# Kernel optimization log

Hardware: AMD Instinct MI355X
Metric: run time of the kernel (lower is better)

Reference implementation:

```python
import jax, jax.numpy as jnp
import numpy as np

N = 50000      # nodes
E = 800000     # edges (avg degree 16)
F_IN = 128
# (d_in, d_out) for the 9 GCNConv layers with width=256, n_layers=3
DIMS = [(128, 128), (128, 192), (192, 256), (256, 256), (256, 256), (256, 256), (256, 192), (192, 128), (128, 1)]
# ReLU after every conv except loop conv i==n_layers-2 (conv idx 4) and the final conv
RELU = [True, True, True, True, False, True, True, True, False]


def setup_inputs() -> dict:
    key = jax.random.key(0)
    ks = jax.random.split(key, 2 + 2 * len(DIMS))
    inp = {
        "x": jax.random.normal(ks[0], (N, F_IN), dtype=jnp.float32),
        "edge_index": jax.random.randint(ks[1], (2, E), 0, N, dtype=jnp.int64),
    }
    for i, (din, dout) in enumerate(DIMS):
        # Glorot-ish init for weights, small random bias (GCNConv has bias=True)
        inp[f"W{i}"] = jax.random.normal(ks[2 + 2 * i], (din, dout), dtype=jnp.float32) / np.float32(np.sqrt(din))
        inp[f"b{i}"] = jax.random.normal(ks[3 + 2 * i], (dout,), dtype=jnp.float32) * 0.01
    return inp


def _gcn_stack(x, src_f, dst_f, norm, Ws, bs):
    h = x
    for i in range(len(Ws)):
        h = h @ Ws[i]                                  # [N, dout] dense transform first (dout <= din mostly)
        msg = h[src_f] * norm[:, None]                 # gather + edge-normalize  [E+N, dout]
        h = jax.ops.segment_sum(msg, dst_f, num_segments=N) + bs[i]
        if RELU[i]:
            h = jax.nn.relu(h)
        # Dropout layers are identity in eval/inference mode.
    return h


def reference(x, edge_index,
              W0, b0, W1, b1, W2, b2, W3, b3, W4, b4, W5, b5, W6, b6, W7, b7, W8, b8):
    src, dst = edge_index[0], edge_index[1]
    loop = jnp.arange(N, dtype=src.dtype)
    # GCNConv default: add self loops, symmetric normalization D^{-1/2}(A+I)D^{-1/2}
    src_f = jnp.concatenate([src, loop])
    dst_f = jnp.concatenate([dst, loop])
    deg = jax.ops.segment_sum(jnp.ones(E + N, dtype=x.dtype), dst_f, num_segments=N)
    dinv = jax.lax.rsqrt(jnp.maximum(deg, 1.0))        # deg >= 1 thanks to self loops
    norm = dinv[src_f] * dinv[dst_f]                   # per-edge coefficient [E+N]
    Ws = [W0, W1, W2, W3, W4, W5, W6, W7, W8]
    bs = [b0, b1, b2, b3, b4, b5, b6, b7, b8]
    return _gcn_stack(x, src_f, dst_f, norm, Ws, bs)   # [N, 1]
```

## Files before the change

### kernel.cpp

```cpp
#include <hip/hip_runtime.h>


#define TPB 256

using bf16x8 = __attribute__((ext_vector_type(8))) __bf16;
using f32x4  = __attribute__((ext_vector_type(4))) float;
using f32x2  = __attribute__((ext_vector_type(2))) float;

__device__ __forceinline__ unsigned bf16rne(float x) {
    unsigned u = __float_as_uint(x);
    return (u + 0x7fffu + ((u >> 16) & 1u)) >> 16;
}

__device__ __forceinline__ f32x2 bl2(unsigned u) {
    return (f32x2){__uint_as_float(u << 16), __uint_as_float(u & 0xffff0000u)};
}

__device__ __forceinline__ void stage16(const unsigned short* g, unsigned short* l) {
#if __has_builtin(__builtin_amdgcn_global_load_lds)
    __builtin_amdgcn_global_load_lds((const __attribute__((address_space(1))) void*)g,
                                     (__attribute__((address_space(3))) void*)l, 16, 0, 0);
#else
    *(uint4*)((char*)l + (threadIdx.x & 63) * 16) = *(const uint4*)g;
#endif
}


__global__ void zinit_kernel(int* cnt, int n) {
    int i = blockIdx.x * blockDim.x + threadIdx.x;
    if (i < n) cnt[i] = 0;
}

__global__ void count_kernel(const int* __restrict__ dst, int* __restrict__ cnt,
                             int* __restrict__ rank, int E) {
    int e = blockIdx.x * blockDim.x + threadIdx.x;
    if (e < E) rank[e] = atomicAdd(&cnt[dst[e]], 1);
}


__global__ void blockhist_kernel(const int* __restrict__ cnt, int* __restrict__ localRank,
                                 int* __restrict__ hb, float* __restrict__ dinv,
                                 int n, int nb) {
    __shared__ int h[64];
    int t = threadIdx.x;
    if (t < 64) h[t] = 0;
    __syncthreads();
    int i = blockIdx.x * TPB + t;
    if (i < n) {
        int c = cnt[i];
        dinv[i] = rsqrtf((float)(c + 1));
        int d = c; if (d > 63) d = 63;
        localRank[i] = atomicAdd(&h[d], 1);
    }
    __syncthreads();
    if (t < 64) hb[t * nb + blockIdx.x] = h[t];
}

__global__ __launch_bounds__(256) void sortscan_kernel(int* __restrict__ hb, int nb) {
    __shared__ int sh[64 * 256];
    __shared__ int tot[64], base[64];
    int t = threadIdx.x;
    int total = 64 * nb;
    for (int i = t; i < total; i += 256) sh[i] = hb[i];
    __syncthreads();
    if (t < 64) {
        int run = 0;
        for (int b = 0; b < nb; b++) {
            int v = sh[t * nb + b];
            sh[t * nb + b] = run;
            run += v;
        }
        tot[t] = run;
    }
    __syncthreads();
    if (t == 0) {
        int acc = 0;
        for (int b = 0; b < 64; b++) { base[b] = acc; acc += tot[b]; }
    }
    __syncthreads();
    for (int i = t; i < total; i += 256) hb[i] = sh[i] + base[i / nb];
}

__global__ void scatter2_kernel(const int* __restrict__ cnt,
                                const int* __restrict__ localRank, const int* __restrict__ hb,
                                int* __restrict__ perm, int* __restrict__ pcnt,
                                int* __restrict__ iperm, int n, int nb) {
    int i = blockIdx.x * TPB + threadIdx.x;
    if (i >= n) return;
    int c = cnt[i];
    int d = c; if (d > 63) d = 63;
    int pos = hb[d * nb + blockIdx.x] + localRank[i];
    perm[pos] = i;
    pcnt[pos] = c;
    iperm[i] = pos;
}

__global__ void scan1_kernel(const int* __restrict__ pcnt, int* __restrict__ prowp2,
                             int* __restrict__ bsums, int n) {
    __shared__ int sh[TPB];
    int t = threadIdx.x;
    int i = blockIdx.x * TPB + t;
    int v = (i < n) ? (pcnt[i] + 1) : 0;
    sh[t] = v;
    __syncthreads();
    for (int off = 1; off < TPB; off <<= 1) {
        int x = (t >= off) ? sh[t - off] : 0;
        __syncthreads();
        sh[t] += x;
        __syncthreads();
    }
    if (i < n) prowp2[i] = sh[t] - v;
    if (t == TPB - 1) bsums[blockIdx.x] = sh[t];
}

__global__ void scan2_kernel(int* __restrict__ bsums, int nb) {
    __shared__ int sh[TPB];
    int t = threadIdx.x;
    int v = (t < nb) ? bsums[t] : 0;
    sh[t] = v;
    __syncthreads();
    for (int off = 1; off < TPB; off <<= 1) {
        int x = (t >= off) ? sh[t - off] : 0;
        __syncthreads();
        sh[t] += x;
        __syncthreads();
    }
    if (t < nb) bsums[t] = sh[t] - v;
}

__global__ void scan3_kernel(int* __restrict__ rowp, const int* __restrict__ bsums, int n) {
    int i = blockIdx.x * TPB + threadIdx.x;
    if (i < n) rowp[i] += bsums[blockIdx.x];
}

__global__ void rowo_kernel(const int* __restrict__ iperm, const int* __restrict__ prowp2,
                            int* __restrict__ rowo, int n) {
    int i = blockIdx.x * TPB + threadIdx.x;
    if (i < n) rowo[i] = prowp2[iperm[i]];
}

__global__ void fillself_kernel(const int* __restrict__ src, const int* __restrict__ dst,
                                const int* __restrict__ rank,
                                const float* __restrict__ dinv,
                                const int* __restrict__ rowo,
                                const int* __restrict__ cnt,
                                unsigned* __restrict__ edges2, int E, int n) {
    int id = blockIdx.x * blockDim.x + threadIdx.x;
    if (id < E) {
        int s = src[id], d = dst[id];
        int pos = rowo[d] + rank[id];
        edges2[pos] = (unsigned)s | (bf16rne(dinv[s] * dinv[d]) << 16);
    } else if (id < E + n) {
        int i = id - E;
        float dv = dinv[i];
        edges2[rowo[i] + cnt[i]] = (unsigned)i | (bf16rne(dv * dv) << 16);
    }
}


struct WPtrs { const float* p[8]; };

__global__ void wt_all_kernel(WPtrs wp, unsigned short* __restrict__ Wts) {
    const int cum[9] = {0, 16384, 40960, 90112, 155648, 221184, 286720, 335872, 360448};
    const int Ns[8] = {128, 192, 256, 256, 256, 256, 192, 128};
    const int Ks[8] = {128, 128, 192, 256, 256, 256, 256, 192};
    int id = blockIdx.x * blockDim.x + threadIdx.x;
    if (id >= 360448) return;
    int L = 0;
#pragma unroll
    for (int t = 1; t < 8; t++) if (id >= cum[t]) L = t;
    int lid = id - cum[L];
    int N = Ns[L], K = Ks[L];
    int k = lid / N, n = lid - k * N;
    Wts[cum[L] + n * K + k] = (unsigned short)bf16rne(wp.p[L][lid]);
}

__global__ void cvt_bf16_kernel(const float* __restrict__ in, unsigned short* __restrict__ out,
                                int n4) {
    int i = blockIdx.x * blockDim.x + threadIdx.x;
    if (i >= n4) return;
    float4 v = ((const float4*)in)[i];
    uint2 o;
    o.x = bf16rne(v.x) | (bf16rne(v.y) << 16);
    o.y = bf16rne(v.z) | (bf16rne(v.w) << 16);
    ((uint2*)out)[i] = o;
}


__global__ __launch_bounds__(256) void gemm_mfma_kernel(
    const unsigned short* __restrict__ A, const unsigned short* __restrict__ Wt,
    const float* __restrict__ bias, unsigned short* __restrict__ C,
    int M, int K, int Nc, int doBias, int doRelu, int outChunked) {
    __shared__ unsigned short Qb[128 * 64];
    __shared__ unsigned short Pb[128 * 64];
    int tid = threadIdx.x;
    int l = tid & 63, w = tid >> 6;
    int node0 = blockIdx.x * 128, feat0 = blockIdx.y * 128;

    f32x4 acc[4][4];
#pragma unroll
    for (int i = 0; i < 4; i++)
#pragma unroll
        for (int j = 0; j < 4; j++) acc[i][j] = (f32x4){0.f, 0.f, 0.f, 0.f};

    const unsigned short* gQ[4];
    const unsigned short* gP[4];
    unsigned short* lQ[4];
    unsigned short* lP[4];
#pragma unroll
    for (int h = 0; h < 4; h++) {
        int slot = tid + h * 256;
        int r = slot >> 3, q = slot & 7;
        int qg = q ^ (r & 7);
        int nd = node0 + r; if (nd > M - 1) nd = M - 1;
        int ft = feat0 + r; if (ft > Nc - 1) ft = Nc - 1;
        gQ[h] = A + (size_t)nd * K + qg * 8;
        gP[h] = Wt + (size_t)ft * K + qg * 8;
        lQ[h] = Qb + (size_t)(w * 64 + h * 256) * 8;
        lP[h] = Pb + (size_t)(w * 64 + h * 256) * 8;
    }

    int q4 = l >> 4, m16 = l & 15;
    int featHalf = w & 1, nodeHalf = w >> 1;
    int rP0 = featHalf * 64 + m16;
    int rQ0 = nodeHalf * 64 + m16;
    int sw = m16 & 7;

    for (int k0 = 0; k0 < K; k0 += 64) {
        __syncthreads();
#pragma unroll
        for (int h = 0; h < 4; h++) {
            stage16(gQ[h] + k0, lQ[h]);
            stage16(gP[h] + k0, lP[h]);
        }
        __syncthreads();
#pragma unroll
        for (int ko = 0; ko < 2; ko++) {
            bf16x8 pf[4], qf[4];
#pragma unroll
            for (int i = 0; i < 4; i++)
                pf[i] = *(const bf16x8*)(Pb + (rP0 + i * 16) * 64 + ((ko * 4 + q4) ^ sw) * 8);
#pragma unroll
            for (int j = 0; j < 4; j++)
                qf[j] = *(const bf16x8*)(Qb + (rQ0 + j * 16) * 64 + ((ko * 4 + q4) ^ sw) * 8);
#pragma unroll
            for (int i = 0; i < 4; i++)
#pragma unroll
                for (int j = 0; j < 4; j++)
                    acc[i][j] = __builtin_amdgcn_mfma_f32_16x16x32_bf16(pf[i], qf[j],
                                                                        acc[i][j], 0, 0, 0);
        }
    }

#pragma unroll
    for (int i = 0; i < 4; i++) {
        int gf0 = feat0 + featHalf * 64 + i * 16 + q4 * 4;
        if (gf0 >= Nc) continue;
        float4 bv = make_float4(0.f, 0.f, 0.f, 0.f);
        if (doBias) bv = *(const float4*)(bias + gf0);
        size_t cb = outChunked ? ((size_t)(gf0 >> 6) * ((size_t)M * 64) + (gf0 & 63))
                               : (size_t)gf0;
#pragma unroll
        for (int j = 0; j < 4; j++) {
            int gn = node0 + nodeHalf * 64 + j * 16 + m16;
            if (gn >= M) continue;
            f32x4 v = acc[i][j];
            float x0 = v[0] + bv.x, x1 = v[1] + bv.y;
            float x2 = v[2] + bv.z, x3 = v[3] + bv.w;
            if (doRelu) {
                x0 = fmaxf(x0, 0.f); x1 = fmaxf(x1, 0.f);
                x2 = fmaxf(x2, 0.f); x3 = fmaxf(x3, 0.f);
            }
            uint2 o;
            o.x = bf16rne(x0) | (bf16rne(x1) << 16);
            o.y = bf16rne(x2) | (bf16rne(x3) << 16);
            size_t off = outChunked ? (cb + (size_t)gn * 64) : (cb + (size_t)gn * Nc);
            *(uint2*)(C + off) = o;
        }
    }
}

__global__ void gemv128_bf16_kernel(const unsigned short* __restrict__ A,
                                    const float* __restrict__ w,
                                    float* __restrict__ out, int M) {
    int wid = (blockIdx.x * blockDim.x + threadIdx.x) >> 6;
    int lane = threadIdx.x & 63;
    if (wid >= M) return;
    const unsigned short* a = A + (size_t)wid * 128;
    float a0 = __uint_as_float((unsigned)a[lane] << 16);
    float a1 = __uint_as_float((unsigned)a[lane + 64] << 16);
    float s = a0 * w[lane] + a1 * w[lane + 64];
#pragma unroll
    for (int off = 32; off > 0; off >>= 1) s += __shfl_down(s, off);
    if (lane == 0) out[wid] = s;
}


__global__ __launch_bounds__(256) void agg_group_kernel(
    const uint4* __restrict__ in, const int* __restrict__ prowp2,
    const int* __restrict__ pcnt, const int* __restrict__ perm,
    const unsigned* __restrict__ edges2,
    const float* __restrict__ bias, uint4* __restrict__ out,
    int Q, int upx, int ngPerUnit, int NG, int n_nodes, int rowVec4,
    int doBias, int doRelu, int outChunked) {
    int xcd = blockIdx.x & 7;
    int slot = blockIdx.x >> 3;
    int u = slot / ngPerUnit;
    int ngIdx = slot - u * ngPerUnit;
    int unit = xcd * upx + u;
    int chunk = unit / Q;
    int q = unit - chunk * Q;
    int ng = ngIdx * Q + q;
    if (ng >= NG) return;
    ng = NG - 1 - ng;

    int wave = threadIdx.x >> 6;
    int lane = threadIdx.x & 63;
    int group = lane >> 3, fl = lane & 7;
    int gb = lane & ~7;
    int i = ng * 32 + wave * 8 + group;
    if (i >= n_nodes) return;

    const uint4* sf = in + (size_t)chunk * n_nodes * 8 + fl;
    int s0 = prowp2[i];
    int c = pcnt[i] + 1;
    int node = perm[i];
    const unsigned* ep = edges2 + s0;

    f32x2 acc[2][4];
#pragma unroll
    for (int k = 0; k < 2; k++)
#pragma unroll
        for (int m = 0; m < 4; m++) acc[k][m] = (f32x2){0.f, 0.f};

    unsigned ew = (fl < c) ? ep[fl] : 0u;
    unsigned eA[4]; uint4 pA[4];
#pragma unroll
    for (int j = 0; j < 4; j++) eA[j] = (unsigned)__shfl((int)ew, gb + j);
#pragma unroll
    for (int j = 0; j < 4; j++) pA[j] = sf[(size_t)(eA[j] & 0xffffu) * 8];

    for (int base = 0; base < c; base += 8) {
        unsigned ewn = (base + 8 + fl < c) ? ep[base + 8 + fl] : 0u;
        unsigned eB[4]; uint4 pB[4];
#pragma unroll
        for (int j = 0; j < 4; j++) eB[j] = (unsigned)__shfl((int)ew, gb + 4 + j);
#pragma unroll
        for (int j = 0; j < 4; j++) pB[j] = sf[(size_t)(eB[j] & 0xffffu) * 8];
#pragma unroll
        for (int j = 0; j < 4; j++) {
            float wgt = __uint_as_float(eA[j] & 0xffff0000u);
            f32x2 w2 = {wgt, wgt};
            int k = j & 1;
            acc[k][0] += w2 * bl2(pA[j].x);
            acc[k][1] += w2 * bl2(pA[j].y);
            acc[k][2] += w2 * bl2(pA[j].z);
            acc[k][3] += w2 * bl2(pA[j].w);
        }
#pragma unroll
        for (int j = 0; j < 4; j++) eA[j] = (unsigned)__shfl((int)ewn, gb + j);
#pragma unroll
        for (int j = 0; j < 4; j++) pA[j] = sf[(size_t)(eA[j] & 0xffffu) * 8];
#pragma unroll
        for (int j = 0; j < 4; j++) {
            float wgt = __uint_as_float(eB[j] & 0xffff0000u);
            f32x2 w2 = {wgt, wgt};
            int k = j & 1;
            acc[k][0] += w2 * bl2(pB[j].x);
            acc[k][1] += w2 * bl2(pB[j].y);
            acc[k][2] += w2 * bl2(pB[j].z);
            acc[k][3] += w2 * bl2(pB[j].w);
        }
        ew = ewn;
    }
    f32x2 s[4];
#pragma unroll
    for (int m = 0; m < 4; m++) s[m] = acc[0][m] + acc[1][m];

    if (doBias) {
        const float* bp = bias + chunk * 64 + fl * 8;
        float4 b0 = *(const float4*)bp;
        float4 b1 = *(const float4*)(bp + 4);
        s[0] += (f32x2){b0.x, b0.y};
        s[1] += (f32x2){b0.z, b0.w};
        s[2] += (f32x2){b1.x, b1.y};
        s[3] += (f32x2){b1.z, b1.w};
    }
    if (doRelu) {
#pragma unroll
        for (int m = 0; m < 4; m++) {
            s[m][0] = fmaxf(s[m][0], 0.f);
            s[m][1] = fmaxf(s[m][1], 0.f);
        }
    }
    uint4 o;
    o.x = bf16rne(s[0][0]) | (bf16rne(s[0][1]) << 16);
    o.y = bf16rne(s[1][0]) | (bf16rne(s[1][1]) << 16);
    o.z = bf16rne(s[2][0]) | (bf16rne(s[2][1]) << 16);
    o.w = bf16rne(s[3][0]) | (bf16rne(s[3][1]) << 16);
    size_t oi = outChunked ? ((size_t)chunk * n_nodes * 8 + (size_t)node * 8 + fl)
                           : ((size_t)node * rowVec4 + chunk * 8 + fl);
    out[oi] = o;
}

__global__ void agg1_kernel(const float* __restrict__ in, const int* __restrict__ prowp2,
                            const int* __restrict__ pcnt, const int* __restrict__ perm,
                            const unsigned* __restrict__ edges2,
                            const float* __restrict__ bias, float* __restrict__ out,
                            int n_nodes) {
    int n = blockIdx.x * blockDim.x + threadIdx.x;
    if (n >= n_nodes) return;
    float acc = 0.f;
    int s0 = prowp2[n];
    int c = pcnt[n] + 1;
    for (int j = 0; j < c; j++) {
        unsigned e = edges2[s0 + j];
        acc += __uint_as_float(e & 0xffff0000u) * in[e & 0xffffu];
    }
    acc += bias[0];
    out[perm[n]] = acc;
}


extern "C" void kernel_launch(void* const* d_in, const int* in_sizes, int n_in,
                              void* d_out, int out_size, void* d_ws, size_t ws_size,
                              hipStream_t stream) {
    const float* x = (const float*)d_in[0];
    const int* ei = (const int*)d_in[1];
    const int Nn = in_sizes[0] / 128;
    const int E = in_sizes[1] / 2;
    const int* src = ei;
    const int* dst = ei + E;

    char* ws = (char*)d_ws;
    size_t off = 0;
    auto alloc = [&](size_t bytes) -> char* {
        char* p = ws + off;
        off = (off + bytes + 255) & ~(size_t)255;
        return p;
    };
    int* cnt = (int*)alloc((size_t)Nn * 4);
    int* rank = (int*)alloc((size_t)E * 4);
    int* bsums = (int*)alloc(1024);
    float* dinv = (float*)alloc((size_t)Nn * 4);
    int* localRank = (int*)alloc((size_t)Nn * 4);
    int* hb = (int*)alloc((size_t)64 * 256 * 4);
    int* perm = (int*)alloc((size_t)Nn * 4);
    int* pcnt = (int*)alloc((size_t)Nn * 4);
    int* iperm = (int*)alloc((size_t)Nn * 4);
    int* prowp2 = (int*)alloc((size_t)Nn * 4);
    int* rowo = (int*)alloc((size_t)Nn * 4);
    unsigned* edges2 = (unsigned*)alloc((size_t)(E + Nn + 64) * 4);
    unsigned short* T = (unsigned short*)alloc((size_t)Nn * 256 * 2);
    unsigned short* H = (unsigned short*)alloc((size_t)Nn * 256 * 2);
    unsigned short* Bx = (unsigned short*)alloc((size_t)Nn * 128 * 2);
    float* F = (float*)alloc((size_t)Nn * 4);
    unsigned short* Wts = (unsigned short*)alloc((size_t)400000 * 2);
    (void)ws_size;

    const int dims[9][2] = {{128,128},{128,192},{192,256},{256,256},{256,256},
                            {256,256},{256,192},{192,128},{128,1}};
    unsigned short* Wt[8];
    {
        size_t o = 0;
        for (int i = 0; i < 8; i++) { Wt[i] = Wts + o; o += (size_t)dims[i][0] * dims[i][1]; }
    }

    int nbN = (Nn + TPB - 1) / TPB;
    int nbE = (E + TPB - 1) / TPB;
    int nbEN = (E + Nn + TPB - 1) / TPB;

    zinit_kernel<<<nbN, TPB, 0, stream>>>(cnt, Nn);
    count_kernel<<<nbE, TPB, 0, stream>>>(dst, cnt, rank, E);
    blockhist_kernel<<<nbN, TPB, 0, stream>>>(cnt, localRank, hb, dinv, Nn, nbN);
    sortscan_kernel<<<1, 256, 0, stream>>>(hb, nbN);
    scatter2_kernel<<<nbN, TPB, 0, stream>>>(cnt, localRank, hb, perm, pcnt, iperm,
                                             Nn, nbN);
    scan1_kernel<<<nbN, TPB, 0, stream>>>(pcnt, prowp2, bsums, Nn);
    scan2_kernel<<<1, TPB, 0, stream>>>(bsums, nbN);
    scan3_kernel<<<nbN, TPB, 0, stream>>>(prowp2, bsums, Nn);
    rowo_kernel<<<nbN, TPB, 0, stream>>>(iperm, prowp2, rowo, Nn);
    fillself_kernel<<<nbEN, TPB, 0, stream>>>(src, dst, rank, dinv, rowo, cnt,
                                              edges2, E, Nn);

    WPtrs wp;
    for (int i = 0; i < 8; i++) wp.p[i] = (const float*)d_in[2 + 2 * i];
    wt_all_kernel<<<(360448 + TPB - 1) / TPB, TPB, 0, stream>>>(wp, Wts);
    cvt_bf16_kernel<<<(Nn * 32 + TPB - 1) / TPB, TPB, 0, stream>>>(x, Bx, Nn * 32);

    auto gemm = [&](const unsigned short* A, int i, unsigned short* C, int K, int Nc,
                    int doBias, int doRelu, int outChunked) {
        const float* b = (const float*)d_in[3 + 2 * i];
        dim3 grid((Nn + 127) / 128, (Nc + 127) / 128);
        gemm_mfma_kernel<<<grid, 256, 0, stream>>>(A, Wt[i], b, C, Nn, K, Nc,
                                                   doBias, doRelu, outChunked);
    };
    int NG = (Nn + 31) / 32;
    auto agg = [&](const unsigned short* inb, unsigned short* outb, int w, int i,
                   int doBias, int doRelu, int outChunked) {
        int nch = w / 64;
        int Q = (nch == 4) ? 2 : (nch == 3) ? 8 : 4;
        int upx = nch * Q / 8;
        int ngPerUnit = (NG + Q - 1) / Q;
        int blocksPerXcd = upx * ngPerUnit;
        const float* b = (const float*)d_in[3 + 2 * i];
        agg_group_kernel<<<blocksPerXcd * 8, 256, 0, stream>>>(
            (const uint4*)inb, prowp2, pcnt, perm, edges2, b, (uint4*)outb,
            Q, upx, ngPerUnit, NG, Nn, w / 8, doBias, doRelu, outChunked);
    };

    gemm(Bx, 0, T, 128, 128, 0, 0, 1);
    agg(T, H, 128, 0, 1, 1, 1);
    agg(H, T, 128, 1, 0, 0, 0);
    gemm(T, 1, H, 128, 192, 1, 1, 1);
    agg(H, T, 192, 2, 0, 0, 0);
    gemm(T, 2, H, 192, 256, 1, 1, 0);
    gemm(H, 3, T, 256, 256, 0, 0, 1);
    agg(T, H, 256, 3, 1, 1, 0);
    gemm(H, 4, T, 256, 256, 0, 0, 1);
    agg(T, H, 256, 4, 1, 0, 0);
    gemm(H, 5, T, 256, 256, 0, 0, 1);
    agg(T, H, 256, 5, 1, 1, 0);
    gemm(H, 6, T, 256, 192, 0, 0, 1);
    agg(T, H, 192, 6, 1, 1, 0);
    gemm(H, 7, T, 192, 128, 0, 0, 1);
    agg(T, H, 128, 7, 1, 1, 0);
    gemv128_bf16_kernel<<<(Nn + 3) / 4, 256, 0, stream>>>(H, (const float*)d_in[2 + 16],
                                                          F, Nn);
    agg1_kernel<<<nbN, TPB, 0, stream>>>(F, prowp2, pcnt, perm, edges2,
                                         (const float*)d_in[3 + 16], (float*)d_out, Nn);
}
```

Measured before the change: 581.7 us.

## Add 128-wide chunked aggregation kernel and matching GEMM output layout

Adds an aggregation kernel that processes 128-feature chunks, with 16 lanes per node each loading a full uint4 row segment, in place of 64-feature chunks. GEMMs feeding these aggregations now write a 128-wide chunked layout. The aim is fewer passes over the edge list per layer and wider contiguous gathers per edge. The 192-wide layers keep the old kernel. The trade-off is more registers per lane and a different work split across XCDs.

```diff
diff --git a/kernel.cpp b/kernel.cpp
--- a/kernel.cpp
+++ b/kernel.cpp
@@ -190,7 +190,7 @@
 __global__ __launch_bounds__(256) void gemm_mfma_kernel(
     const unsigned short* __restrict__ A, const unsigned short* __restrict__ Wt,
     const float* __restrict__ bias, unsigned short* __restrict__ C,
-    int M, int K, int Nc, int doBias, int doRelu, int outChunked) {
+    int M, int K, int Nc, int doBias, int doRelu, int outMode) {
     __shared__ unsigned short Qb[128 * 64];
     __shared__ unsigned short Pb[128 * 64];
     int tid = threadIdx.x;
@@ -258,8 +258,10 @@
         if (gf0 >= Nc) continue;
         float4 bv = make_float4(0.f, 0.f, 0.f, 0.f);
         if (doBias) bv = *(const float4*)(bias + gf0);
-        size_t cb = outChunked ? ((size_t)(gf0 >> 6) * ((size_t)M * 64) + (gf0 & 63))
-                               : (size_t)gf0;
+        size_t cb; int stride;
+        if (outMode == 2) { cb = (size_t)(gf0 >> 7) * ((size_t)M * 128) + (gf0 & 127); stride = 128; }
+        else if (outMode == 1) { cb = (size_t)(gf0 >> 6) * ((size_t)M * 64) + (gf0 & 63); stride = 64; }
+        else { cb = (size_t)gf0; stride = Nc; }
 #pragma unroll
         for (int j = 0; j < 4; j++) {
             int gn = node0 + nodeHalf * 64 + j * 16 + m16;
@@ -274,7 +276,7 @@
             uint2 o;
             o.x = bf16rne(x0) | (bf16rne(x1) << 16);
             o.y = bf16rne(x2) | (bf16rne(x3) << 16);
-            size_t off = outChunked ? (cb + (size_t)gn * 64) : (cb + (size_t)gn * Nc);
+            size_t off = cb + (size_t)gn * stride;
             *(uint2*)(C + off) = o;
         }
     }
@@ -400,6 +402,108 @@
     o.w = bf16rne(s[3][0]) | (bf16rne(s[3][1]) << 16);
     size_t oi = outChunked ? ((size_t)chunk * n_nodes * 8 + (size_t)node * 8 + fl)
                            : ((size_t)node * rowVec4 + chunk * 8 + fl);
+    out[oi] = o;
+}
+
+
+__global__ __launch_bounds__(256) void agg128_kernel(
+    const uint4* __restrict__ in, const int* __restrict__ prowp2,
+    const int* __restrict__ pcnt, const int* __restrict__ perm,
+    const unsigned* __restrict__ edges2,
+    const float* __restrict__ bias, uint4* __restrict__ out,
+    int Q, int upx, int ngPerUnit, int NG, int n_nodes, int rowVec4,
+    int doBias, int doRelu, int outChunked) {
+    int xcd = blockIdx.x & 7;
+    int slot = blockIdx.x >> 3;
+    int u = slot / ngPerUnit;
+    int ngIdx = slot - u * ngPerUnit;
+    int unit = xcd * upx + u;
+    int chunk = unit / Q;
+    int q = unit - chunk * Q;
+    int ng = ngIdx * Q + q;
+    if (ng >= NG) return;
+    ng = NG - 1 - ng;
+
+    int wave = threadIdx.x >> 6;
+    int lane = threadIdx.x & 63;
+    int group = lane >> 4, fl = lane & 15;
+    int gb = lane & ~15;
+    int i = ng * 16 + wave * 4 + group;
+    if (i >= n_nodes) return;
+
+    const uint4* sf = in + (size_t)chunk * n_nodes * 16 + fl;
+    int s0 = prowp2[i];
+    int c = pcnt[i] + 1;
+    int node = perm[i];
+    const unsigned* ep = edges2 + s0;
+
+    f32x2 acc[2][4];
+#pragma unroll
+    for (int k = 0; k < 2; k++)
+#pragma unroll
+        for (int m = 0; m < 4; m++) acc[k][m] = (f32x2){0.f, 0.f};
+
+    unsigned ew = (fl < c) ? ep[fl] : 0u;
+    unsigned eA[4]; uint4 pA[4];
+#pragma unroll
+    for (int j = 0; j < 4; j++) eA[j] = (unsigned)__shfl((int)ew, gb + j);
+#pragma unroll
+    for (int j = 0; j < 4; j++) pA[j] = sf[(size_t)(eA[j] & 0xffffu) * 16];
+
+    for (int base = 0; base < c; base += 16) {
+        unsigned ewn = (base + 16 + fl < c) ? ep[base + 16 + fl] : 0u;
+#pragma unroll
+        for (int sb = 0; sb < 4; sb++) {
+            unsigned esrc = (sb < 3) ? ew : ewn;
+            int lsel = (sb + 1) & 3;
+            unsigned eB[4]; uint4 pB[4];
+#pragma unroll
+            for (int j = 0; j < 4; j++)
+                eB[j] = (unsigned)__shfl((int)esrc, gb + lsel * 4 + j);
+#pragma unroll
+            for (int j = 0; j < 4; j++) pB[j] = sf[(size_t)(eB[j] & 0xffffu) * 16];
+#pragma unroll
+            for (int j = 0; j < 4; j++) {
+                float wgt = __uint_as_float(eA[j] & 0xffff0000u);
+                f32x2 w2 = {wgt, wgt};
+                int k = j & 1;
+                acc[k][0] += w2 * bl2(pA[j].x);
+                acc[k][1] += w2 * bl2(pA[j].y);
+                acc[k][2] += w2 * bl2(pA[j].z);
+                acc[k][3] += w2 * bl2(pA[j].w);
+            }
+#pragma unroll
+            for (int j = 0; j < 4; j++) { eA[j] = eB[j]; pA[j] = pB[j]; }
+        }
+        ew = ewn;
+    }
+    f32x2 s[4];
+#pragma unroll
+    for (int m = 0; m < 4; m++) s[m] = acc[0][m] + acc[1][m];
+
+    if (doBias) {
+        const float* bp = bias + chunk * 128 + fl * 8;
+        float4 b0 = *(const float4*)bp;
+        float4 b1 = *(const float4*)(bp + 4);
+        s[0] += (f32x2){b0.x, b0.y};
+        s[1] += (f32x2){b0.z, b0.w};
+        s[2] += (f32x2){b1.x, b1.y};
+        s[3] += (f32x2){b1.z, b1.w};
+    }
+    if (doRelu) {
+#pragma unroll
+        for (int m = 0; m < 4; m++) {
+            s[m][0] = fmaxf(s[m][0], 0.f);
+            s[m][1] = fmaxf(s[m][1], 0.f);
+        }
+    }
+    uint4 o;
+    o.x = bf16rne(s[0][0]) | (bf16rne(s[0][1]) << 16);
+    o.y = bf16rne(s[1][0]) | (bf16rne(s[1][1]) << 16);
+    o.z = bf16rne(s[2][0]) | (bf16rne(s[2][1]) << 16);
+    o.w = bf16rne(s[3][0]) | (bf16rne(s[3][1]) << 16);
+    size_t oi = outChunked ? ((size_t)chunk * n_nodes * 16 + (size_t)node * 16 + fl)
+                           : ((size_t)node * rowVec4 + chunk * 16 + fl);
     out[oi] = o;
 }
 
@@ -489,41 +593,49 @@
     cvt_bf16_kernel<<<(Nn * 32 + TPB - 1) / TPB, TPB, 0, stream>>>(x, Bx, Nn * 32);
 
     auto gemm = [&](const unsigned short* A, int i, unsigned short* C, int K, int Nc,
-                    int doBias, int doRelu, int outChunked) {
+                    int doBias, int doRelu, int outMode) {
         const float* b = (const float*)d_in[3 + 2 * i];
         dim3 grid((Nn + 127) / 128, (Nc + 127) / 128);
         gemm_mfma_kernel<<<grid, 256, 0, stream>>>(A, Wt[i], b, C, Nn, K, Nc,
-                                                   doBias, doRelu, outChunked);
+                                                   doBias, doRelu, outMode);
     };
-    int NG = (Nn + 31) / 32;
+    int NG64 = (Nn + 31) / 32;
+    int NG128 = (Nn + 15) / 16;
     auto agg = [&](const unsigned short* inb, unsigned short* outb, int w, int i,
                    int doBias, int doRelu, int outChunked) {
-        int nch = w / 64;
-        int Q = (nch == 4) ? 2 : (nch == 3) ? 8 : 4;
-        int upx = nch * Q / 8;
-        int ngPerUnit = (NG + Q - 1) / Q;
-        int blocksPerXcd = upx * ngPerUnit;
         const float* b = (const float*)d_in[3 + 2 * i];
-        agg_group_kernel<<<blocksPerXcd * 8, 256, 0, stream>>>(
-            (const uint4*)inb, prowp2, pcnt, perm, edges2, b, (uint4*)outb,
-            Q, upx, ngPerUnit, NG, Nn, w / 8, doBias, doRelu, outChunked);
+        if (w == 192) {
+            int Q = 8, upx = 3;
+            int ngPerUnit = (NG64 + Q - 1) / Q;
+            agg_group_kernel<<<upx * ngPerUnit * 8, 256, 0, stream>>>(
+                (const uint4*)inb, prowp2, pcnt, perm, edges2, b, (uint4*)outb,
+                Q, upx, ngPerUnit, NG64, Nn, w / 8, doBias, doRelu, outChunked);
+        } else {
+            int nch = w / 128;
+            int Q = (nch == 2) ? 4 : 8;
+            int upx = nch * Q / 8;
+            int ngPerUnit = (NG128 + Q - 1) / Q;
+            agg128_kernel<<<upx * ngPerUnit * 8, 256, 0, stream>>>(
+                (const uint4*)inb, prowp2, pcnt, perm, edges2, b, (uint4*)outb,
+                Q, upx, ngPerUnit, NG128, Nn, w / 8, doBias, doRelu, outChunked);
+        }
     };
 
-    gemm(Bx, 0, T, 128, 128, 0, 0, 1);
-    agg(T, H, 128, 0, 1, 1, 1);
+    gemm(Bx, 0, T, 128, 128, 0, 0, 2);
+    agg(T, H, 128, 0, 1, 1, 0);
     agg(H, T, 128, 1, 0, 0, 0);
     gemm(T, 1, H, 128, 192, 1, 1, 1);
     agg(H, T, 192, 2, 0, 0, 0);
     gemm(T, 2, H, 192, 256, 1, 1, 0);
-    gemm(H, 3, T, 256, 256, 0, 0, 1);
+    gemm(H, 3, T, 256, 256, 0, 0, 2);
     agg(T, H, 256, 3, 1, 1, 0);
-    gemm(H, 4, T, 256, 256, 0, 0, 1);
+    gemm(H, 4, T, 256, 256, 0, 0, 2);
     agg(T, H, 256, 4, 1, 0, 0);
-    gemm(H, 5, T, 256, 256, 0, 0, 1);
+    gemm(H, 5, T, 256, 256, 0, 0, 2);
     agg(T, H, 256, 5, 1, 1, 0);
     gemm(H, 6, T, 256, 192, 0, 0, 1);
     agg(T, H, 192, 6, 1, 1, 0);
-    gemm(H, 7, T, 192, 128, 0, 0, 1);
+    gemm(H, 7, T, 192, 128, 0, 0, 2);
     agg(T, H, 128, 7, 1, 1, 0);
     gemv128_bf16_kernel<<<(Nn + 3) / 4, 256, 0, stream>>>(H, (const float*)d_in[2 + 16],
                                                           F, Nn);
```

New measurement: 635.8 us. 1.09x slower.
